# Kernel tuning notes

Measured on AMD Instinct MI355X. Metric: run time of the kernel, lower is better.

Reference implementation:

```python
import jax, jax.numpy as jnp
import numpy as np
from math import sqrt

RATIOS = [0.5, 1.0, 2.0]
SCALES = [128.0, 256.0, 512.0]
STRIDE = 16
NA = 9  # len(RATIOS) * len(SCALES)


def _anchor_template():
    # matches RPNHead.__init__: center at stride/2, w = s/sqrt(r), h = s*sqrt(r)
    t = np.zeros((NA, 4), np.float32)
    for ri, r in enumerate(RATIOS):
        for si, s in enumerate(SCALES):
            i = ri * len(RATIOS) + si
            sr = sqrt(r)
            t[i] = [STRIDE / 2.0, STRIDE / 2.0, s / sr, s * sr]
    return jnp.asarray(t)


def _conv(x, w, b, pad):
    y = jax.lax.conv_general_dilated(
        x, w, window_strides=(1, 1), padding=[(pad, pad), (pad, pad)],
        dimension_numbers=('NCHW', 'OIHW', 'NCHW'))
    return y + b[None, :, None, None]


def setup_inputs() -> dict:
    key = jax.random.key(0)
    ks = jax.random.split(key, 5)
    B, C, H, W = 8, 512, 64, 64
    return {
        'feature_maps': jax.random.normal(ks[0], (B, C, H, W), jnp.float32),
        'img_size': jnp.ones((B, 2), jnp.int32) * 1024,  # (width, height) per image
        'conv_w': jax.random.normal(ks[1], (512, 512, 3, 3), jnp.float32) * 0.01,
        'conv_b': jnp.zeros((512,), jnp.float32),
        'cls_w': jax.random.normal(ks[2], (2 * NA, 512, 1, 1), jnp.float32) * 0.01,
        'cls_b': jnp.zeros((2 * NA,), jnp.float32),
        'reg_w': jax.random.normal(ks[3], (4 * NA, 512, 1, 1), jnp.float32) * 0.01,
        'reg_b': jnp.zeros((4 * NA,), jnp.float32),
    }


def reference(feature_maps, img_size, conv_w, conv_b, cls_w, cls_b, reg_w, reg_b):
    f = jax.nn.relu(_conv(feature_maps, conv_w, conv_b, 1))  # [B,512,H,W]
    B, _, H, W = f.shape
    # heads, NCHW -> NHWC, split anchor dim
    cls = _conv(f, cls_w, cls_b, 0).transpose(0, 2, 3, 1).reshape(B, H, W, NA, 2)
    reg = _conv(f, reg_w, reg_b, 0).transpose(0, 2, 3, 1).reshape(B, H, W, NA, 4)

    # generate_anchors (eval mode: anchors_ignore stays zero)
    tmpl = _anchor_template()  # [NA,4] xywh
    gy, gx = jnp.meshgrid(jnp.arange(H), jnp.arange(W), indexing='ij')
    center = jnp.stack([gx, gy], axis=-1).astype(jnp.float32) * STRIDE  # [H,W,2] (x,y)
    axy = tmpl[None, None, :, :2] + center[:, :, None, :]               # [H,W,NA,2]
    awh = jnp.broadcast_to(tmpl[None, None, :, 2:], (H, W, NA, 2))
    anchors = jnp.concatenate([axy, awh], axis=-1).reshape(-1, 4)       # [A,4]

    A = anchors.shape[0]
    reg = reg.reshape(B, A, 4)
    cls_scores = cls.reshape(B, A, 2)

    # anchor2bbox: inverse of the delta encoding in loss()
    ax, ay, aw, ah = anchors[:, 0], anchors[:, 1], anchors[:, 2], anchors[:, 3]
    px = ax[None, :] + reg[..., 0] * aw[None, :]
    py = ay[None, :] + reg[..., 1] * ah[None, :]
    pw = aw[None, :] * jnp.exp(reg[..., 2])
    ph = ah[None, :] * jnp.exp(reg[..., 3])
    imw = img_size[:, 0:1].astype(jnp.float32)
    imh = img_size[:, 1:2].astype(jnp.float32)
    x1 = jnp.clip(px - pw / 2, 0.0, imw)
    y1 = jnp.clip(py - ph / 2, 0.0, imh)
    x2 = jnp.clip(px + pw / 2, 0.0, imw)
    y2 = jnp.clip(py + ph / 2, 0.0, imh)
    proposals = jnp.stack([x1, y1, x2, y2], axis=-1)  # [B,A,4]

    anchors_ignore = jnp.zeros((B, A), jnp.int32)
    return (proposals, cls_scores, anchors_ignore)
```

## Files before the change

### kernel.cpp

```cpp
#include <hip/hip_runtime.h>
#include <hip/hip_bf16.h>
#include <stdint.h>

typedef __attribute__((ext_vector_type(4))) float f32x4;
typedef __attribute__((ext_vector_type(8))) short short8;

#define NB 8
#define NC 512
#define HP 66
#define WP 66
#define NPOS 32768
#define KTOT 4608
#define NT 144

#define XP_ELEMS (NB*HP*WP*NC)
#define WR_ELEMS (NC*KTOT)
#define WC2_ELEMS (64*NC)
#define PROP_OFF 0
#define CLS_OFF  1179648
#define ANCH_OFF 1769472
#define A_PER_B  36864

__device__ __forceinline__ short bf16bits(float v) {
    __hip_bfloat16 b = __float2bfloat16(v);
    return *reinterpret_cast<short*>(&b);
}
__device__ __forceinline__ void gload16(const short* g, short* l) {
    __builtin_amdgcn_global_load_lds(
        (const __attribute__((address_space(1))) unsigned int*)g,
        (__attribute__((address_space(3))) unsigned int*)l, 16, 0, 0);
}
#define BARRIER() asm volatile("s_barrier" ::: "memory")
#define VMCNT4()  asm volatile("s_waitcnt vmcnt(4)" ::: "memory")
#define VMCNT0()  asm volatile("s_waitcnt vmcnt(0)" ::: "memory")

__global__ void prep_input(const float* __restrict__ x, short* __restrict__ Xp) {
    __shared__ float t[64][65];
    const int pb = blockIdx.x, cb = blockIdx.y, b = blockIdx.z;
    const int tid = threadIdx.x;
    const int tx = tid & 63, ty = tid >> 6;
    const float* src = x + ((size_t)(b*NC + cb*64))*4096 + pb*64;
#pragma unroll
    for (int r = 0; r < 16; ++r) {
        int ch = ty + r*4;
        t[ch][tx] = src[(size_t)ch*4096 + tx];
    }
    __syncthreads();
#pragma unroll
    for (int rr = 0; rr < 2; ++rr) {
        int item = tid + rr*256;
        int pl = item >> 3, ck = item & 7;
        short8 v;
#pragma unroll
        for (int e = 0; e < 8; ++e) v[e] = bf16bits(t[ck*8+e][pl]);
        *(short8*)&Xp[((size_t)((b*HP + pb + 1)*WP) + (pl + 1))*NC + cb*64 + ck*8] = v;
    }
}

__global__ void prep_w(const float* __restrict__ w, short* __restrict__ Wr) {
    __shared__ float t[4608];
    const int o = blockIdx.x;
    const int tid = threadIdx.x;
    const float* src = w + (size_t)o*4608;
    for (int i = tid; i < 4608; i += 256) t[i] = src[i];
    __syncthreads();
#pragma unroll
    for (int k = 0; k < 9; ++k) {
#pragma unroll
        for (int c = 0; c < 2; ++c) {
            int ci = tid + c*256;
            Wr[(size_t)o*4608 + k*512 + ci] = bf16bits(t[ci*9 + k]);
        }
    }
}

__global__ void prep_misc(const float* __restrict__ cls_w, const float* __restrict__ reg_w,
                          short* __restrict__ Wc2, short* __restrict__ Xp,
                          float* __restrict__ out) {
    const int bid = blockIdx.x, tid = threadIdx.x;
    if (bid < 128) {
        int t = bid*256 + tid;
        int row = t >> 9, ci = t & 511;
        float v = 0.f;
        if (row < 18)      v = cls_w[row*NC + ci];
        else if (row < 54) v = reg_w[(row-18)*NC + ci];
        Wc2[t] = bf16bits(v);
    } else if (bid < 648) {
        int idx = (bid-128)*256 + tid;
        int b = idx / 16640;
        int rem = idx - b*16640;
        int r = rem >> 6, g = rem & 63;
        int h, w;
        if      (r < 66)  { h = 0;       w = r; }
        else if (r < 132) { h = 65;      w = r - 66; }
        else if (r < 196) { h = r - 131; w = 0; }
        else              { h = r - 195; w = 65; }
        short8 z = (short8){0,0,0,0,0,0,0,0};
        *(short8*)&Xp[((size_t)((b*HP + h)*WP) + w)*NC + g*8] = z;
    } else {
        int idx = (bid-648)*256 + tid;
        ((float4*)(out + ANCH_OFF))[idx] = make_float4(0.f,0.f,0.f,0.f);
    }
}

__device__ const float AW_T[9] = {
    181.01933598375618f, 362.03867196751236f, 724.0773439350247f,
    128.f, 256.f, 512.f,
    90.50966799187809f, 181.01933598375618f, 362.03867196751236f };
__device__ const float AH_T[9] = {
    90.50966799187809f, 181.01933598375618f, 362.03867196751236f,
    128.f, 256.f, 512.f,
    181.01933598375618f, 362.03867196751236f, 724.0773439350247f };

__launch_bounds__(512, 2)
__global__ void conv_fused(const short* __restrict__ Xp, const short* __restrict__ Wr,
                           const float* __restrict__ bias, const short* __restrict__ Wc2,
                           const float* __restrict__ cls_b, const float* __restrict__ reg_b,
                           const int* __restrict__ img, float* __restrict__ out) {
    extern __shared__ short lds[];
    short* Ab0 = lds;            short* Ab1 = lds + 4096;
    short* Bb0 = lds + 8192;     short* Bb1 = lds + 8192 + 16384;
    short* Bb2 = lds + 8192 + 32768;
    short* ABUF[2] = {Ab0, Ab1};
    short* BBUF[3] = {Bb0, Bb1, Bb2};

    const int tid = threadIdx.x;
    const int lane = tid & 63, wv = tid >> 6;
    const int bid = blockIdx.x;
    const int wg = (bid & 7) * 32 + (bid >> 3);
    const int pbase = wg * 128;
    const int wm = wv >> 2, wn = wv & 3;
    const int l15 = lane & 15, lg = lane >> 4;

    const int G = ((tid & 3) - (tid >> 3)) & 3;
    int aoff;
    {
        int p = pbase + (tid >> 2);
        int b = p >> 12, h = (p >> 6) & 63, w = p & 63;
        aoff = ((b*HP + h)*WP + w)*NC + G*8;
    }
    const int boff = (tid >> 2)*KTOT + G*8;
    const int sdst = tid*8;

    const int sigma = (((lg + ((l15 >> 1) & 3)) & 3)) * 8;

    f32x4 acc[4][8];
#pragma unroll
    for (int i = 0; i < 4; ++i)
#pragma unroll
        for (int j = 0; j < 8; ++j) acc[i][j] = (f32x4){0.f,0.f,0.f,0.f};

    short8 af_[4], bf_[8];

    auto stageA = [&](int t, short* dst) {
        int seg = t >> 4;
        int dh = seg/3, dw = seg - dh*3;
        gload16(Xp + aoff + (dh*WP + dw)*NC + (t & 15)*32, dst + sdst);
    };
    auto stageB2 = [&](int t, short* dst, int q0) {
#pragma unroll
        for (int q = q0; q < q0+2; ++q)
            gload16(Wr + boff + q*128*KTOT + t*32, dst + q*4096 + sdst);
    };
    auto phA = [&](short* Ar, short* Br, bool sA, short* Aw, bool sB, short* Bw, int t) {
#pragma unroll
        for (int j = 0; j < 8; ++j)
            bf_[j] = *(const short8*)(Br + (wn*128 + j*16 + l15)*32 + sigma);
#pragma unroll
        for (int ii = 0; ii < 2; ++ii)
            af_[ii] = *(const short8*)(Ar + (wm*64 + ii*16 + l15)*32 + sigma);
        if (sA) stageA(t+1, Aw);
        if (sB) stageB2(t+2, Bw, 0);
        BARRIER();
        __builtin_amdgcn_s_setprio(1);
#pragma unroll
        for (int ii = 0; ii < 2; ++ii)
#pragma unroll
            for (int j = 0; j < 8; ++j)
                acc[ii][j] = __builtin_amdgcn_mfma_f32_16x16x32_bf16(
                    af_[ii], bf_[j], acc[ii][j], 0, 0, 0);
        __builtin_amdgcn_s_setprio(0);
        BARRIER();
    };
    auto phB = [&](short* Ar, bool sB, short* Bw, int t, int vm) {
#pragma unroll
        for (int ii = 2; ii < 4; ++ii)
            af_[ii] = *(const short8*)(Ar + (wm*64 + ii*16 + l15)*32 + sigma);
        if (sB) stageB2(t+2, Bw, 2);
        BARRIER();
        __builtin_amdgcn_s_setprio(1);
#pragma unroll
        for (int ii = 2; ii < 4; ++ii)
#pragma unroll
            for (int j = 0; j < 8; ++j)
                acc[ii][j] = __builtin_amdgcn_mfma_f32_16x16x32_bf16(
                    af_[ii], bf_[j], acc[ii][j], 0, 0, 0);
        __builtin_amdgcn_s_setprio(0);
        if (vm == 4) { VMCNT4(); } else if (vm == 0) { VMCNT0(); }
        BARRIER();
    };

    stageB2(0, Bb0, 0); stageB2(0, Bb0, 2);
    stageA(0, Ab0);
    stageB2(1, Bb1, 0); stageB2(1, Bb1, 2);
    VMCNT4(); BARRIER();

#pragma unroll 1
    for (int itt = 0; itt < 23; ++itt) {
        const int t0 = itt*6;
#pragma unroll
        for (int c = 0; c < 6; ++c) {
            const int t = t0 + c;
            phA(ABUF[c&1], BBUF[c%3], true, ABUF[(c+1)&1], true, BBUF[(c+2)%3], t);
            phB(ABUF[c&1], true, BBUF[(c+2)%3], t, 4);
        }
    }
    {
#pragma unroll
        for (int c = 0; c < 6; ++c) {
            const int t = 138 + c;
            const bool sA = (c < 5), sB = (c < 4);
            const int vm = (c < 4) ? 4 : (c == 4 ? 0 : -1);
            phA(ABUF[c&1], BBUF[c%3], sA, ABUF[(c+1)&1], sB, BBUF[(c+2)%3], t);
            phB(ABUF[c&1], sB, BBUF[(c+2)%3], t, vm);
        }
    }

#pragma unroll
    for (int j = 0; j < 8; ++j) {
        const int co = wn*128 + j*16 + l15;
        const float bb = bias[co];
        const int g64 = co >> 3, e = co & 7;
#pragma unroll
        for (int i = 0; i < 4; ++i) {
#pragma unroll
            for (int r = 0; r < 4; ++r) {
                const int prow = wm*64 + i*16 + lg*4 + r;
                float v = acc[i][j][r] + bb;
                v = v > 0.f ? v : 0.f;
                const int slot = (g64 & 56) | ((g64 ^ prow) & 7);
                lds[prow*512 + slot*8 + e] = bf16bits(v);
            }
        }
    }
    __syncthreads();

    f32x4 acc2[4];
#pragma unroll
    for (int j = 0; j < 4; ++j) acc2[j] = (f32x4){0.f,0.f,0.f,0.f};
    const int hrow = wv*16 + l15;
#pragma unroll
    for (int k0 = 0; k0 < 16; ++k0) {
        const int g64 = k0*4 + lg;
        const int slot = (g64 & 56) | ((g64 ^ hrow) & 7);
        short8 a2 = *(const short8*)&lds[hrow*512 + slot*8];
#pragma unroll
        for (int j = 0; j < 4; ++j) {
            short8 b2 = *(const short8*)&Wc2[(size_t)(j*16 + l15)*NC + k0*32 + lg*8];
            acc2[j] = __builtin_amdgcn_mfma_f32_16x16x32_bf16(a2, b2, acc2[j], 0, 0, 0);
        }
    }
    __syncthreads();

    float* sm = (float*)lds;
    const int crow0 = wv*16 + lg*4;
#pragma unroll
    for (int j = 0; j < 4; ++j)
#pragma unroll
        for (int r = 0; r < 4; ++r)
            sm[(crow0 + r)*65 + j*16 + l15] = acc2[j][r];
    __syncthreads();

    for (int item = tid; item < 1152; item += 512) {
        int pl = item / 9, a = item - pl*9;
        int p = pbase + pl;
        int b = p >> 12, h = (p >> 6) & 63, w = p & 63;
        float c0 = sm[pl*65 + a*2 + 0] + cls_b[a*2 + 0];
        float c1 = sm[pl*65 + a*2 + 1] + cls_b[a*2 + 1];
        float r0 = sm[pl*65 + 18 + a*4 + 0] + reg_b[a*4 + 0];
        float r1 = sm[pl*65 + 18 + a*4 + 1] + reg_b[a*4 + 1];
        float r2 = sm[pl*65 + 18 + a*4 + 2] + reg_b[a*4 + 2];
        float r3 = sm[pl*65 + 18 + a*4 + 3] + reg_b[a*4 + 3];
        float aw = AW_T[a], ah = AH_T[a];
        float ax = 8.f + 16.f*w, ay = 8.f + 16.f*h;
        float px = ax + r0*aw,  py = ay + r1*ah;
        float pw = aw*__expf(r2), ph = ah*__expf(r3);
        float imw = (float)img[b*2 + 0], imh = (float)img[b*2 + 1];
        float x1 = fminf(fmaxf(px - 0.5f*pw, 0.f), imw);
        float y1 = fminf(fmaxf(py - 0.5f*ph, 0.f), imh);
        float x2 = fminf(fmaxf(px + 0.5f*pw, 0.f), imw);
        float y2 = fminf(fmaxf(py + 0.5f*ph, 0.f), imh);
        int ag = (h*64 + w)*9 + a;
        float4* prop = (float4*)(out + PROP_OFF + ((size_t)b*A_PER_B + ag)*4);
        *prop = make_float4(x1, y1, x2, y2);
        float2* cs = (float2*)(out + CLS_OFF + ((size_t)b*A_PER_B + ag)*2);
        *cs = make_float2(c0, c1);
    }
}

extern "C" void kernel_launch(void* const* d_in, const int* in_sizes, int n_in,
                              void* d_out, int out_size, void* d_ws, size_t ws_size,
                              hipStream_t stream) {
    const float* x      = (const float*)d_in[0];
    const int*   img    = (const int*)  d_in[1];
    const float* conv_w = (const float*)d_in[2];
    const float* conv_b = (const float*)d_in[3];
    const float* cls_w  = (const float*)d_in[4];
    const float* cls_b  = (const float*)d_in[5];
    const float* reg_w  = (const float*)d_in[6];
    const float* reg_b  = (const float*)d_in[7];
    float* out = (float*)d_out;

    short* Xp  = (short*)d_ws;
    short* Wr  = Xp  + XP_ELEMS;
    short* Wc2 = Wr  + WR_ELEMS;

    prep_misc<<<936, 256, 0, stream>>>(cls_w, reg_w, Wc2, Xp, out);
    prep_input<<<dim3(64,8,8), 256, 0, stream>>>(x, Xp);
    prep_w <<<512, 256, 0, stream>>>(conv_w, Wr);

    hipFuncSetAttribute((const void*)conv_fused,
                        hipFuncAttributeMaxDynamicSharedMemorySize, 131072);
    conv_fused<<<256, 512, 131072, stream>>>(Xp, Wr, conv_b, Wc2,
                                             cls_b, reg_b, img, out);
}
```

Before: 265.9 us.

## Merge prep kernels into one launch and triple-buffer the A tile

The three preprocessing kernels (input transpose to padded NHWC bf16, weight reorder, misc head weights/padding zeroing) are folded into one launch dispatched by block index, which removes two kernel launches and the gaps between them. In the main conv loop the A (activation) tile moves from double to triple buffering and is prefetched two steps ahead, the same distance as B, with the wait count raised to match. This gives the activation loads more latency slack at the cost of extra LDS, and the loop is restructured into 3-step unrolled groups with an explicit tail.

New measurement: 266.2 us. No clear change (+0.1%).

```diff
diff --git a/kernel.cpp b/kernel.cpp
--- a/kernel.cpp
+++ b/kernel.cpp
@@ -31,75 +31,72 @@
         (__attribute__((address_space(3))) unsigned int*)l, 16, 0, 0);
 }
 #define BARRIER() asm volatile("s_barrier" ::: "memory")
-#define VMCNT4()  asm volatile("s_waitcnt vmcnt(4)" ::: "memory")
+#define VMCNT5()  asm volatile("s_waitcnt vmcnt(5)" ::: "memory")
 #define VMCNT0()  asm volatile("s_waitcnt vmcnt(0)" ::: "memory")
 
-__global__ void prep_input(const float* __restrict__ x, short* __restrict__ Xp) {
-    __shared__ float t[64][65];
-    const int pb = blockIdx.x, cb = blockIdx.y, b = blockIdx.z;
-    const int tid = threadIdx.x;
-    const int tx = tid & 63, ty = tid >> 6;
-    const float* src = x + ((size_t)(b*NC + cb*64))*4096 + pb*64;
-#pragma unroll
-    for (int r = 0; r < 16; ++r) {
-        int ch = ty + r*4;
-        t[ch][tx] = src[(size_t)ch*4096 + tx];
-    }
-    __syncthreads();
-#pragma unroll
-    for (int rr = 0; rr < 2; ++rr) {
-        int item = tid + rr*256;
-        int pl = item >> 3, ck = item & 7;
-        short8 v;
-#pragma unroll
-        for (int e = 0; e < 8; ++e) v[e] = bf16bits(t[ck*8+e][pl]);
-        *(short8*)&Xp[((size_t)((b*HP + pb + 1)*WP) + (pl + 1))*NC + cb*64 + ck*8] = v;
-    }
-}
-
-__global__ void prep_w(const float* __restrict__ w, short* __restrict__ Wr) {
-    __shared__ float t[4608];
-    const int o = blockIdx.x;
-    const int tid = threadIdx.x;
-    const float* src = w + (size_t)o*4608;
-    for (int i = tid; i < 4608; i += 256) t[i] = src[i];
-    __syncthreads();
-#pragma unroll
-    for (int k = 0; k < 9; ++k) {
-#pragma unroll
-        for (int c = 0; c < 2; ++c) {
-            int ci = tid + c*256;
-            Wr[(size_t)o*4608 + k*512 + ci] = bf16bits(t[ci*9 + k]);
-        }
-    }
-}
-
-__global__ void prep_misc(const float* __restrict__ cls_w, const float* __restrict__ reg_w,
-                          short* __restrict__ Wc2, short* __restrict__ Xp,
-                          float* __restrict__ out) {
+__global__ void prep_all(const float* __restrict__ x, const float* __restrict__ conv_w,
+                         const float* __restrict__ cls_w, const float* __restrict__ reg_w,
+                         short* __restrict__ Wr, short* __restrict__ Wc2,
+                         short* __restrict__ Xp, float* __restrict__ out) {
+    __shared__ float smem[4608];
     const int bid = blockIdx.x, tid = threadIdx.x;
-    if (bid < 128) {
-        int t = bid*256 + tid;
-        int row = t >> 9, ci = t & 511;
-        float v = 0.f;
-        if (row < 18)      v = cls_w[row*NC + ci];
-        else if (row < 54) v = reg_w[(row-18)*NC + ci];
-        Wc2[t] = bf16bits(v);
-    } else if (bid < 648) {
-        int idx = (bid-128)*256 + tid;
-        int b = idx / 16640;
-        int rem = idx - b*16640;
-        int r = rem >> 6, g = rem & 63;
-        int h, w;
-        if      (r < 66)  { h = 0;       w = r; }
-        else if (r < 132) { h = 65;      w = r - 66; }
-        else if (r < 196) { h = r - 131; w = 0; }
-        else              { h = r - 195; w = 65; }
-        short8 z = (short8){0,0,0,0,0,0,0,0};
-        *(short8*)&Xp[((size_t)((b*HP + h)*WP) + w)*NC + g*8] = z;
+    if (bid < 4096) {
+        float (*t)[65] = (float(*)[65])smem;
+        const int pb = bid & 63, cb = (bid >> 6) & 7, b = bid >> 9;
+        const int tx = tid & 63, ty = tid >> 6;
+        const float* src = x + ((size_t)(b*NC + cb*64))*4096 + pb*64;
+#pragma unroll
+        for (int r = 0; r < 16; ++r) {
+            int ch = ty + r*4;
+            t[ch][tx] = src[(size_t)ch*4096 + tx];
+        }
+        __syncthreads();
+#pragma unroll
+        for (int rr = 0; rr < 2; ++rr) {
+            int item = tid + rr*256;
+            int pl = item >> 3, ck = item & 7;
+            short8 v;
+#pragma unroll
+            for (int e = 0; e < 8; ++e) v[e] = bf16bits(t[ck*8+e][pl]);
+            *(short8*)&Xp[((size_t)((b*HP + pb + 1)*WP) + (pl + 1))*NC + cb*64 + ck*8] = v;
+        }
+    } else if (bid < 4608) {
+        const int o = bid - 4096;
+        const float* src = conv_w + (size_t)o*4608;
+        for (int i = tid; i < 4608; i += 256) smem[i] = src[i];
+        __syncthreads();
+#pragma unroll
+        for (int k = 0; k < 9; ++k)
+#pragma unroll
+            for (int c = 0; c < 2; ++c) {
+                int ci = tid + c*256;
+                Wr[(size_t)o*4608 + k*512 + ci] = bf16bits(smem[ci*9 + k]);
+            }
     } else {
-        int idx = (bid-648)*256 + tid;
-        ((float4*)(out + ANCH_OFF))[idx] = make_float4(0.f,0.f,0.f,0.f);
+        const int m = bid - 4608;
+        if (m < 128) {
+            int t = m*256 + tid;
+            int row = t >> 9, ci = t & 511;
+            float v = 0.f;
+            if (row < 18)      v = cls_w[row*NC + ci];
+            else if (row < 54) v = reg_w[(row-18)*NC + ci];
+            Wc2[t] = bf16bits(v);
+        } else if (m < 648) {
+            int idx = (m-128)*256 + tid;
+            int b = idx / 16640;
+            int rem = idx - b*16640;
+            int r = rem >> 6, g = rem & 63;
+            int h, w;
+            if      (r < 66)  { h = 0;       w = r; }
+            else if (r < 132) { h = 65;      w = r - 66; }
+            else if (r < 196) { h = r - 131; w = 0; }
+            else              { h = r - 195; w = 65; }
+            short8 z = (short8){0,0,0,0,0,0,0,0};
+            *(short8*)&Xp[((size_t)((b*HP + h)*WP) + w)*NC + g*8] = z;
+        } else {
+            int idx = (m-648)*256 + tid;
+            ((float4*)(out + ANCH_OFF))[idx] = make_float4(0.f,0.f,0.f,0.f);
+        }
     }
 }
 
@@ -118,11 +115,8 @@
                            const float* __restrict__ cls_b, const float* __restrict__ reg_b,
                            const int* __restrict__ img, float* __restrict__ out) {
     extern __shared__ short lds[];
-    short* Ab0 = lds;            short* Ab1 = lds + 4096;
-    short* Bb0 = lds + 8192;     short* Bb1 = lds + 8192 + 16384;
-    short* Bb2 = lds + 8192 + 32768;
-    short* ABUF[2] = {Ab0, Ab1};
-    short* BBUF[3] = {Bb0, Bb1, Bb2};
+    short* ABUF[3] = {lds, lds + 4096, lds + 8192};
+    short* BBUF[3] = {lds + 12288, lds + 12288 + 16384, lds + 12288 + 32768};
 
     const int tid = threadIdx.x;
     const int lane = tid & 63, wv = tid >> 6;
@@ -162,14 +156,13 @@
         for (int q = q0; q < q0+2; ++q)
             gload16(Wr + boff + q*128*KTOT + t*32, dst + q*4096 + sdst);
     };
-    auto phA = [&](short* Ar, short* Br, bool sA, short* Aw, bool sB, short* Bw, int t) {
+    auto phA = [&](short* Ar, short* Br, bool sB, short* Bw, int t) {
 #pragma unroll
         for (int j = 0; j < 8; ++j)
             bf_[j] = *(const short8*)(Br + (wn*128 + j*16 + l15)*32 + sigma);
 #pragma unroll
         for (int ii = 0; ii < 2; ++ii)
             af_[ii] = *(const short8*)(Ar + (wm*64 + ii*16 + l15)*32 + sigma);
-        if (sA) stageA(t+1, Aw);
         if (sB) stageB2(t+2, Bw, 0);
         BARRIER();
         __builtin_amdgcn_s_setprio(1);
@@ -182,10 +175,11 @@
         __builtin_amdgcn_s_setprio(0);
         BARRIER();
     };
-    auto phB = [&](short* Ar, bool sB, short* Bw, int t, int vm) {
+    auto phB = [&](short* Ar, bool sA, short* Aw, bool sB, short* Bw, int t, int vm) {
 #pragma unroll
         for (int ii = 2; ii < 4; ++ii)
             af_[ii] = *(const short8*)(Ar + (wm*64 + ii*16 + l15)*32 + sigma);
+        if (sA) stageA(t+2, Aw);
         if (sB) stageB2(t+2, Bw, 2);
         BARRIER();
         __builtin_amdgcn_s_setprio(1);
@@ -196,35 +190,34 @@
                 acc[ii][j] = __builtin_amdgcn_mfma_f32_16x16x32_bf16(
                     af_[ii], bf_[j], acc[ii][j], 0, 0, 0);
         __builtin_amdgcn_s_setprio(0);
-        if (vm == 4) { VMCNT4(); } else if (vm == 0) { VMCNT0(); }
+        if (vm == 5) { VMCNT5(); } else if (vm == 0) { VMCNT0(); }
         BARRIER();
     };
 
-    stageB2(0, Bb0, 0); stageB2(0, Bb0, 2);
-    stageA(0, Ab0);
-    stageB2(1, Bb1, 0); stageB2(1, Bb1, 2);
-    VMCNT4(); BARRIER();
+    stageB2(0, BBUF[0], 0); stageB2(0, BBUF[0], 2);
+    stageA(0, ABUF[0]);
+    stageB2(1, BBUF[1], 0);
+    stageA(1, ABUF[1]);
+    stageB2(1, BBUF[1], 2);
+    VMCNT5(); BARRIER();
 
 #pragma unroll 1
-    for (int itt = 0; itt < 23; ++itt) {
-        const int t0 = itt*6;
-#pragma unroll
-        for (int c = 0; c < 6; ++c) {
+    for (int itt = 0; itt < 47; ++itt) {
+        const int t0 = itt*3;
+#pragma unroll
+        for (int c = 0; c < 3; ++c) {
             const int t = t0 + c;
-            phA(ABUF[c&1], BBUF[c%3], true, ABUF[(c+1)&1], true, BBUF[(c+2)%3], t);
-            phB(ABUF[c&1], true, BBUF[(c+2)%3], t, 4);
-        }
-    }
-    {
-#pragma unroll
-        for (int c = 0; c < 6; ++c) {
-            const int t = 138 + c;
-            const bool sA = (c < 5), sB = (c < 4);
-            const int vm = (c < 4) ? 4 : (c == 4 ? 0 : -1);
-            phA(ABUF[c&1], BBUF[c%3], sA, ABUF[(c+1)&1], sB, BBUF[(c+2)%3], t);
-            phB(ABUF[c&1], sB, BBUF[(c+2)%3], t, vm);
-        }
-    }
+            phA(ABUF[c], BBUF[c], true, BBUF[(c+2)%3], t);
+            phB(ABUF[c], true, ABUF[(c+2)%3], true, BBUF[(c+2)%3], t, 5);
+        }
+    }
+    phA(ABUF[0], BBUF[0], true, BBUF[2], 141);
+    phB(ABUF[0], true, ABUF[2], true, BBUF[2], 141, 5);
+    phA(ABUF[1], BBUF[1], false, BBUF[0], 142);
+    phB(ABUF[1], false, ABUF[0], false, BBUF[0], 142, 0);
+    phA(ABUF[2], BBUF[2], false, BBUF[0], 143);
+    phB(ABUF[2], false, ABUF[0], false, BBUF[0], 143, -1);
+    __syncthreads();
 
 #pragma unroll
     for (int j = 0; j < 8; ++j) {
@@ -315,9 +308,7 @@
     short* Wr  = Xp  + XP_ELEMS;
     short* Wc2 = Wr  + WR_ELEMS;
 
-    prep_misc<<<936, 256, 0, stream>>>(cls_w, reg_w, Wc2, Xp, out);
-    prep_input<<<dim3(64,8,8), 256, 0, stream>>>(x, Xp);
-    prep_w <<<512, 256, 0, stream>>>(conv_w, Wr);
+    prep_all<<<5544, 256, 0, stream>>>(x, conv_w, cls_w, reg_w, Wr, Wc2, Xp, out);
 
     hipFuncSetAttribute((const void*)conv_fused,
                         hipFuncAttributeMaxDynamicSharedMemorySize, 131072);
```
